# Kernel optimization log

Hardware: AMD Instinct MI355X
Metric: run time of the kernel (lower is better)

The kernel has to match this reference:

```python
import jax, jax.numpy as jnp
import numpy as np

V_TH = 1.0
LENS, SCALE, HIGHT, GAMMA = 0.5, 6.0, 0.15, 0.5  # MultiGaussian surrogate constants (DH-SNN)


def _gauss(x, mu, sigma):
    return jnp.exp(-((x - mu) ** 2) / (2.0 * sigma ** 2)) / (jnp.sqrt(2.0 * jnp.pi) * sigma)


@jax.custom_vjp
def spike_fn(x):
    return (x > 0).astype(x.dtype)


def _spike_fwd(x):
    return spike_fn(x), x


def _spike_bwd(x, g):
    sg = GAMMA * (_gauss(x, 0.0, LENS) * (1.0 + HIGHT)
                  - _gauss(x, LENS, SCALE * LENS) * HIGHT
                  - _gauss(x, -LENS, SCALE * LENS) * HIGHT)
    return (g * sg,)


spike_fn.defvjp(_spike_fwd, _spike_bwd)


def setup_inputs() -> dict:
    key = jax.random.key(0)
    ks = jax.random.split(key, 12)
    B, T, I, H, O = 128, 784, 512, 512, 10
    xavier_in = lambda k, sh: jax.random.normal(k, sh, jnp.float32) * jnp.sqrt(2.0 / (sh[0] + sh[1]))
    return {
        'input_data': jax.random.normal(ks[0], (B, T, I), jnp.float32),
        'W1': xavier_in(ks[1], (H, I)),
        'b1': jnp.zeros((H,), jnp.float32),
        'W2': xavier_in(ks[2], (H, I)),
        'b2': jnp.zeros((H,), jnp.float32),
        'tau_m': jax.random.uniform(ks[3], (H,), jnp.float32, 0.0, 4.0),
        'tau_n1': jax.random.uniform(ks[4], (H,), jnp.float32, 2.0, 6.0),
        'tau_n2': jax.random.uniform(ks[5], (H,), jnp.float32, -4.0, 0.0),
        'Wr': xavier_in(ks[6], (O, H)),
        'br': jnp.zeros((O,), jnp.float32),
        'mem0': jax.random.uniform(ks[7], (B, H), jnp.float32),
        'spike0': jax.random.uniform(ks[8], (B, H), jnp.float32),
    }


def reference(input_data, W1, b1, W2, b2, tau_m, tau_n1, tau_n2, Wr, br, mem0, spike0):
    # Batched branch projections for all timesteps (big GEMMs, done once)
    d1_all = jnp.einsum('bti,hi->bth', input_data, W1) + b1  # [B,T,H]
    d2_all = jnp.einsum('bti,hi->bth', input_data, W2) + b2

    alpha = jax.nn.sigmoid(tau_m)    # membrane decay
    beta1 = jax.nn.sigmoid(tau_n1)   # branch-1 dendritic decay
    beta2 = jax.nn.sigmoid(tau_n2)   # branch-2 dendritic decay

    B, H = mem0.shape
    d1_init = jnp.zeros((B, H), input_data.dtype)
    d2_init = jnp.zeros((B, H), input_data.dtype)

    def step(carry, xs):
        mem, spk, d1, d2 = carry
        d1_t, d2_t = xs
        d1 = beta1 * d1 + (1.0 - beta1) * d1_t
        d2 = beta2 * d2 + (1.0 - beta2) * d2_t
        total = d1 + d2
        mem = mem * alpha + (1.0 - alpha) * total - V_TH * spk
        spk = spike_fn(mem - V_TH)
        return (mem, spk, d1, d2), spk

    xs = (jnp.swapaxes(d1_all, 0, 1), jnp.swapaxes(d2_all, 0, 1))  # [T,B,H]
    _, spikes = jax.lax.scan(step, (mem0, spike0, d1_init, d2_init), xs)
    spikes = jnp.swapaxes(spikes, 0, 1)  # [B,T,H]
    out = jnp.einsum('bth,oh->bto', spikes, Wr) + br  # readout per timestep
    return out
```

## Files before the change

kernel.cpp:

```cpp
#include <hip/hip_runtime.h>
#include <cmath>

#define HD 512
#define IN 512
#define TT 784
#define BB 128
#define MH 50176

typedef short short8 __attribute__((ext_vector_type(8)));
typedef unsigned short ushort8 __attribute__((ext_vector_type(8)));
typedef float floatx4 __attribute__((ext_vector_type(4)));

#define GLDS(gp, lp) __builtin_amdgcn_global_load_lds( \
    (const __attribute__((address_space(1))) void*)(gp), \
    (__attribute__((address_space(3))) void*)(lp), 16, 0, 0)

__device__ __forceinline__ unsigned short bf16_rne(float x) {
    unsigned u = __float_as_uint(x);
    unsigned r = u + 0x7FFFu + ((u >> 16) & 1u);
    return (unsigned short)(r >> 16);
}
__device__ __forceinline__ float bf16_f(unsigned short s) {
    return __uint_as_float(((unsigned)s) << 16);
}

__global__ __launch_bounds__(256) void split3(
    const float* __restrict__ src, unsigned short* __restrict__ p1,
    unsigned short* __restrict__ p2, unsigned short* __restrict__ p3, long n8)
{
    long g = (long)blockIdx.x * 256 + threadIdx.x;
    if (g >= n8) return;
    const float* xp = src + g * 8;
    ushort8 o1, o2, o3;
#pragma unroll
    for (int j = 0; j < 8; ++j) {
        float x = xp[j];
        unsigned short s1 = bf16_rne(x);
        float r1 = x - bf16_f(s1);
        unsigned short s2 = bf16_rne(r1);
        float r2 = r1 - bf16_f(s2);
        unsigned short s3 = bf16_rne(r2);
        o1[j] = s1; o2[j] = s2; o3[j] = s3;
    }
    *(ushort8*)(p1 + g * 8) = o1;
    *(ushort8*)(p2 + g * 8) = o2;
    *(ushort8*)(p3 + g * 8) = o3;
}

__global__ __launch_bounds__(256, 2) void gemm_bf16x3(
    const unsigned short* __restrict__ Xp,
    const unsigned short* __restrict__ Wp,
    const float* __restrict__ b1, const float* __restrict__ b2,
    float* __restrict__ d1buf, float* __restrict__ d2buf)
{
    __shared__ unsigned short lds[6][128][32];
    unsigned short* lflat = &lds[0][0][0];
    const int tid  = threadIdx.x;
    const int lane = tid & 63;
    const int w    = tid >> 6;
    const int pn = blockIdx.x & 7;
    const int pm = blockIdx.x >> 3;
    const int m0 = pm * 128;
    const int n0 = pn * 128;

    const unsigned short* gp[12];
    {
        const int rsub = lane >> 2;
        const int csub = (lane & 3) * 8;
#pragma unroll
        for (int j = 0; j < 12; ++j) {
            int seg = w * 12 + j;
            int p = seg >> 3, sub = seg & 7;
            int row16 = sub * 16 + rsub;
            gp[j] = (p < 3)
              ? Xp + ((size_t)p * MH + m0 + row16) * IN + csub
              : Wp + ((size_t)(p - 3) * 1024 + n0 + row16) * IN + csub;
        }
    }

    floatx4 acc[4][4];
#pragma unroll
    for (int i = 0; i < 4; ++i)
#pragma unroll
        for (int j = 0; j < 4; ++j) acc[i][j] = (floatx4){0.f, 0.f, 0.f, 0.f};

    const int wm = w >> 1, wn = w & 1;
    const int c16 = lane & 15;
    const int q8  = (lane >> 4) * 8;

    for (int ks = 0; ks < IN; ks += 32) {
#pragma unroll
        for (int j = 0; j < 12; ++j)
            GLDS(gp[j] + ks, lflat + (size_t)(w * 12 + j) * 512);
        __syncthreads();

        short8 Bf[3][4];
#pragma unroll
        for (int p = 0; p < 3; ++p)
#pragma unroll
            for (int fj = 0; fj < 4; ++fj)
                Bf[p][fj] = *(const short8*)&lds[3 + p][wn * 64 + fj * 16 + c16][q8];

#pragma unroll
        for (int fi = 0; fi < 4; ++fi) {
            const int r = wm * 64 + fi * 16 + c16;
            short8 a1 = *(const short8*)&lds[0][r][q8];
            short8 a2 = *(const short8*)&lds[1][r][q8];
            short8 a3 = *(const short8*)&lds[2][r][q8];
#pragma unroll
            for (int fj = 0; fj < 4; ++fj) {
                floatx4 c = acc[fi][fj];
                c = __builtin_amdgcn_mfma_f32_16x16x32_bf16(a3, Bf[0][fj], c, 0, 0, 0);
                c = __builtin_amdgcn_mfma_f32_16x16x32_bf16(a2, Bf[1][fj], c, 0, 0, 0);
                c = __builtin_amdgcn_mfma_f32_16x16x32_bf16(a1, Bf[2][fj], c, 0, 0, 0);
                c = __builtin_amdgcn_mfma_f32_16x16x32_bf16(a2, Bf[0][fj], c, 0, 0, 0);
                c = __builtin_amdgcn_mfma_f32_16x16x32_bf16(a1, Bf[1][fj], c, 0, 0, 0);
                c = __builtin_amdgcn_mfma_f32_16x16x32_bf16(a1, Bf[0][fj], c, 0, 0, 0);
                acc[fi][fj] = c;
            }
        }
        __syncthreads();
    }

    const int quad = lane >> 4;
    const bool first = (n0 < HD);
    const float* bias = first ? b1 : b2;
    float* obuf = first ? d1buf : d2buf;
    const int nb = n0 & (HD - 1);
    float bv[4];
#pragma unroll
    for (int fj = 0; fj < 4; ++fj) bv[fj] = bias[nb + wn * 64 + fj * 16 + c16];
#pragma unroll
    for (int fi = 0; fi < 4; ++fi) {
#pragma unroll
        for (int fj = 0; fj < 4; ++fj) {
            int n = nb + wn * 64 + fj * 16 + c16;
#pragma unroll
            for (int r = 0; r < 4; ++r) {
                int m = m0 + wm * 64 + fi * 16 + quad * 4 + r;
                obuf[(size_t)m * HD + n] = acc[fi][fj][r] + bv[fj];
            }
        }
    }
}

__global__ __launch_bounds__(64) void scan_half(
    const float* __restrict__ d1buf, const float* __restrict__ d2buf,
    const float* __restrict__ tau_m, const float* __restrict__ tau_n1,
    const float* __restrict__ tau_n2,
    const float* __restrict__ mem0, const float* __restrict__ spike0,
    unsigned short* __restrict__ spikes, int b0)
{
    const int gid = blockIdx.x * 64 + threadIdx.x;
    const int h  = gid & (HD - 1);
    const int bl = gid >> 9;
    const int b  = b0 + bl;
    const float alpha = 1.f / (1.f + expf(-tau_m[h]));
    const float be1   = 1.f / (1.f + expf(-tau_n1[h]));
    const float be2   = 1.f / (1.f + expf(-tau_n2[h]));
    float mem = mem0[b * HD + h];
    float spk = spike0[b * HD + h];
    float d1 = 0.f, d2 = 0.f;
    const float* p1 = d1buf + (size_t)bl * TT * HD + h;
    const float* p2 = d2buf + (size_t)bl * TT * HD + h;
    unsigned short* sp = spikes + (size_t)b * (TT / 16) * HD + h;

#pragma unroll 1
    for (int g = 0; g < TT / 16; ++g) {
        float a1[16], a2[16];
#pragma unroll
        for (int i = 0; i < 16; ++i) {
            a1[i] = p1[(size_t)(g * 16 + i) * HD];
            a2[i] = p2[(size_t)(g * 16 + i) * HD];
        }
        unsigned int word = 0;
#pragma unroll
        for (int i = 0; i < 16; ++i) {
            d1 = be1 * d1 + (1.f - be1) * a1[i];
            d2 = be2 * d2 + (1.f - be2) * a2[i];
            float total = d1 + d2;
            mem = mem * alpha + (1.f - alpha) * total - spk;
            bool fire = (mem - 1.0f) > 0.f;
            spk = fire ? 1.f : 0.f;
            word |= (fire ? 1u : 0u) << i;
        }
        sp[(size_t)g * HD] = (unsigned short)word;
    }
}

__global__ __launch_bounds__(256) void readout(
    const unsigned short* __restrict__ spikes,
    const float* __restrict__ Wr, const float* __restrict__ br,
    float* __restrict__ out)
{
    __shared__ float WrS[10 * HD];
    __shared__ float brS[10];
    const int tid = threadIdx.x;
    for (int i = tid; i < 10 * HD; i += 256) WrS[i] = Wr[i];
    if (tid < 10) brS[tid] = br[tid];
    __syncthreads();

    const int gid = blockIdx.x * 256 + tid;
    const int t = gid % TT;
    const int b = gid / TT;
    const int tw  = t >> 4;
    const int bit = t & 15;
    const unsigned short* row = spikes + ((size_t)b * (TT / 16) + tw) * HD;

    float acc[10];
#pragma unroll
    for (int o = 0; o < 10; ++o) acc[o] = brS[o];

    for (int h = 0; h < HD; ++h) {
        float s = (float)((row[h] >> bit) & 1);
#pragma unroll
        for (int o = 0; o < 10; ++o) acc[o] = fmaf(s, WrS[o * HD + h], acc[o]);
    }
    float* op = out + (size_t)gid * 10;
#pragma unroll
    for (int o = 0; o < 10; ++o) op[o] = acc[o];
}

extern "C" void kernel_launch(void* const* d_in, const int* in_sizes, int n_in,
                              void* d_out, int out_size, void* d_ws, size_t ws_size,
                              hipStream_t stream)
{
    const float* X      = (const float*)d_in[0];
    const float* W1     = (const float*)d_in[1];
    const float* b1     = (const float*)d_in[2];
    const float* W2     = (const float*)d_in[3];
    const float* b2     = (const float*)d_in[4];
    const float* tau_m  = (const float*)d_in[5];
    const float* tau_n1 = (const float*)d_in[6];
    const float* tau_n2 = (const float*)d_in[7];
    const float* Wr     = (const float*)d_in[8];
    const float* br     = (const float*)d_in[9];
    const float* mem0   = (const float*)d_in[10];
    const float* spike0 = (const float*)d_in[11];
    float* out = (float*)d_out;

    char* p = (char*)d_ws;
    unsigned short* Wp = (unsigned short*)p;  p += (size_t)3 * 1024 * IN * 2;
    unsigned short* Xp = (unsigned short*)p;  p += (size_t)3 * MH * IN * 2;
    float* d1buf = (float*)p;                 p += (size_t)MH * HD * 4;
    float* d2buf = (float*)p;                 p += (size_t)MH * HD * 4;
    unsigned short* spikes = (unsigned short*)p;

    const size_t WPS = (size_t)1024 * IN;
    const size_t XPS = (size_t)MH * IN;

    split3<<<dim3(128), dim3(256), 0, stream>>>(
        W1, Wp, Wp + WPS, Wp + 2 * WPS, (long)HD * IN / 8);
    split3<<<dim3(128), dim3(256), 0, stream>>>(
        W2, Wp + (size_t)HD * IN, Wp + WPS + (size_t)HD * IN,
        Wp + 2 * WPS + (size_t)HD * IN, (long)HD * IN / 8);

    for (int half = 0; half < 2; ++half) {
        split3<<<dim3((unsigned)(((long)MH * IN / 8 + 255) / 256)), dim3(256), 0, stream>>>(
            X + (size_t)half * MH * IN, Xp, Xp + XPS, Xp + 2 * XPS, (long)MH * IN / 8);
        gemm_bf16x3<<<dim3(392 * 8), dim3(256), 0, stream>>>(
            Xp, Wp, b1, b2, d1buf, d2buf);
        scan_half<<<dim3(512), dim3(64), 0, stream>>>(
            d1buf, d2buf, tau_m, tau_n1, tau_n2, mem0, spike0,
            spikes, half * 64);
    }
    readout<<<dim3(BB * TT / 256), dim3(256), 0, stream>>>(spikes, Wr, br, out);
}
```

Baseline: 1.120 ms.

## Double-buffer bf16x3 GEMM with 256-row tiles, swizzled LDS and block remap

Result: slower. 1.195 ms (+6.7%).

```diff
diff --git a/kernel.cpp b/kernel.cpp
--- a/kernel.cpp
+++ b/kernel.cpp
@@ -47,34 +47,43 @@
     *(ushort8*)(p3 + g * 8) = o3;
 }
 
-__global__ __launch_bounds__(256, 2) void gemm_bf16x3(
+__global__ __launch_bounds__(512, 2) void gemm_bf16x3_p(
     const unsigned short* __restrict__ Xp,
     const unsigned short* __restrict__ Wp,
     const float* __restrict__ b1, const float* __restrict__ b2,
     float* __restrict__ d1buf, float* __restrict__ d2buf)
 {
-    __shared__ unsigned short lds[6][128][32];
-    unsigned short* lflat = &lds[0][0][0];
+    extern __shared__ unsigned short lds[];
     const int tid  = threadIdx.x;
     const int lane = tid & 63;
     const int w    = tid >> 6;
-    const int pn = blockIdx.x & 7;
-    const int pm = blockIdx.x >> 3;
-    const int m0 = pm * 128;
+
+    const int wg = (blockIdx.x & 7) * 196 + (blockIdx.x >> 3);
+    const int pm = wg >> 3;
+    const int pn = wg & 7;
+    const int m0 = pm * 256;
     const int n0 = pn * 128;
 
-    const unsigned short* gp[12];
+    const unsigned short* gp[9];
+    unsigned loff[9];
     {
         const int rsub = lane >> 2;
-        const int csub = (lane & 3) * 8;
-#pragma unroll
-        for (int j = 0; j < 12; ++j) {
-            int seg = w * 12 + j;
-            int p = seg >> 3, sub = seg & 7;
-            int row16 = sub * 16 + rsub;
-            gp[j] = (p < 3)
-              ? Xp + ((size_t)p * MH + m0 + row16) * IN + csub
-              : Wp + ((size_t)(p - 3) * 1024 + n0 + row16) * IN + csub;
+        const int fst  = ((lane >> 2) & 3) ^ ((lane >> 4) & 3);
+        const int csub = (((lane & 3) ^ fst) * 8);
+#pragma unroll
+        for (int j = 0; j < 9; ++j) {
+            int s = w * 9 + j;
+            const unsigned short* src;
+            if (s < 48) {
+                int p = s >> 4, rb = s & 15;
+                src = Xp + ((size_t)p * MH + m0 + rb * 16 + rsub) * IN + csub;
+            } else {
+                int t2 = s - 48;
+                int p = t2 >> 3, rb = t2 & 7;
+                src = Wp + ((size_t)p * 1024 + n0 + rb * 16 + rsub) * IN + csub;
+            }
+            gp[j] = src;
+            loff[j] = (unsigned)s * 512;
         }
     }
 
@@ -86,27 +95,24 @@
 
     const int wm = w >> 1, wn = w & 1;
     const int c16 = lane & 15;
-    const int q8  = (lane >> 4) * 8;
-
-    for (int ks = 0; ks < IN; ks += 32) {
-#pragma unroll
-        for (int j = 0; j < 12; ++j)
-            GLDS(gp[j] + ks, lflat + (size_t)(w * 12 + j) * 512);
-        __syncthreads();
-
+    const int fr   = (lane & 3) ^ ((lane >> 2) & 3);
+    const int q8s  = (((lane >> 4) ^ fr) & 3) * 8;
+
+    auto compute = [&](int cb) {
         short8 Bf[3][4];
 #pragma unroll
         for (int p = 0; p < 3; ++p)
 #pragma unroll
             for (int fj = 0; fj < 4; ++fj)
-                Bf[p][fj] = *(const short8*)&lds[3 + p][wn * 64 + fj * 16 + c16][q8];
-
+                Bf[p][fj] = *(const short8*)&lds[cb + 24576 + p * 4096 +
+                    (wn * 64 + fj * 16 + c16) * 32 + q8s];
 #pragma unroll
         for (int fi = 0; fi < 4; ++fi) {
-            const int r = wm * 64 + fi * 16 + c16;
-            short8 a1 = *(const short8*)&lds[0][r][q8];
-            short8 a2 = *(const short8*)&lds[1][r][q8];
-            short8 a3 = *(const short8*)&lds[2][r][q8];
+            const int ra = cb + (wm * 64 + fi * 16 + c16) * 32 + q8s;
+            short8 a1 = *(const short8*)&lds[ra];
+            short8 a2 = *(const short8*)&lds[ra + 8192];
+            short8 a3 = *(const short8*)&lds[ra + 16384];
+            __builtin_amdgcn_s_setprio(1);
 #pragma unroll
             for (int fj = 0; fj < 4; ++fj) {
                 floatx4 c = acc[fi][fj];
@@ -118,9 +124,31 @@
                 c = __builtin_amdgcn_mfma_f32_16x16x32_bf16(a1, Bf[0][fj], c, 0, 0, 0);
                 acc[fi][fj] = c;
             }
-        }
-        __syncthreads();
-    }
+            __builtin_amdgcn_s_setprio(0);
+        }
+    };
+
+#pragma unroll
+    for (int j = 0; j < 9; ++j) GLDS(gp[j],      lds + loff[j]);
+#pragma unroll
+    for (int j = 0; j < 9; ++j) GLDS(gp[j] + 32, lds + 36864 + loff[j]);
+
+#pragma unroll 1
+    for (int t = 0; t < 15; ++t) {
+        asm volatile("s_waitcnt vmcnt(9)" ::: "memory");
+        __builtin_amdgcn_s_barrier();
+        const int cb = (t & 1) * 36864;
+        compute(cb);
+        __builtin_amdgcn_s_barrier();
+        if (t < 14) {
+            const int ks = (t + 2) * 32;
+#pragma unroll
+            for (int j = 0; j < 9; ++j) GLDS(gp[j] + ks, lds + cb + loff[j]);
+        }
+    }
+    asm volatile("s_waitcnt vmcnt(0)" ::: "memory");
+    __builtin_amdgcn_s_barrier();
+    compute(36864);
 
     const int quad = lane >> 4;
     const bool first = (n0 < HD);
@@ -239,6 +267,14 @@
     const float* spike0 = (const float*)d_in[11];
     float* out = (float*)d_out;
 
+    static int s_attr = 0;
+    if (!s_attr) {
+        (void)hipFuncSetAttribute(
+            reinterpret_cast<const void*>(gemm_bf16x3_p),
+            hipFuncAttributeMaxDynamicSharedMemorySize, 147456);
+        s_attr = 1;
+    }
+
     char* p = (char*)d_ws;
     unsigned short* Wp = (unsigned short*)p;  p += (size_t)3 * 1024 * IN * 2;
     unsigned short* Xp = (unsigned short*)p;  p += (size_t)3 * MH * IN * 2;
@@ -258,7 +294,7 @@
     for (int half = 0; half < 2; ++half) {
         split3<<<dim3((unsigned)(((long)MH * IN / 8 + 255) / 256)), dim3(256), 0, stream>>>(
             X + (size_t)half * MH * IN, Xp, Xp + XPS, Xp + 2 * XPS, (long)MH * IN / 8);
-        gemm_bf16x3<<<dim3(392 * 8), dim3(256), 0, stream>>>(
+        gemm_bf16x3_p<<<dim3(1568), dim3(512), 147456, stream>>>(
             Xp, Wp, b1, b2, d1buf, d2buf);
         scan_half<<<dim3(512), dim3(64), 0, stream>>>(
             d1buf, d2buf, tau_m, tau_n1, tau_n2, mem0, spike0,
```
